# Performance work log

Measured on AMD Instinct MI355X. Metric: run time of the kernel, lower is better.

## Reference

```python
import jax, jax.numpy as jnp
import numpy as np

B, N, M = 2, 4096, 4096
QUERY_DIM, CONTEXT_DIM = 512, 768
H, D = 8, 64
INNER = H * D


def setup_inputs() -> dict:
    key = jax.random.key(0)
    ks = jax.random.split(key, 8)
    x = jax.random.normal(ks[0], (B, N, QUERY_DIM), dtype=jnp.float32)
    context_tensor = jax.random.normal(ks[1], (B, M, CONTEXT_DIM), dtype=jnp.float32)
    mask = jax.random.randint(ks[2], (B, M), 0, 2) > 0  # bool [B, M]
    s = 0.02
    Wq = jax.random.normal(ks[3], (QUERY_DIM, INNER), dtype=jnp.float32) * s
    Wk = jax.random.normal(ks[4], (CONTEXT_DIM, INNER), dtype=jnp.float32) * s
    Wv = jax.random.normal(ks[5], (CONTEXT_DIM, INNER), dtype=jnp.float32) * s
    Wo = jax.random.normal(ks[6], (INNER, QUERY_DIM), dtype=jnp.float32) * s
    bo = jnp.zeros((QUERY_DIM,), dtype=jnp.float32)
    return {"x": x, "context_tensor": context_tensor, "mask": mask,
            "Wq": Wq, "Wk": Wk, "Wv": Wv, "Wo": Wo, "bo": bo}


def reference(x, context_tensor, mask, Wq, Wk, Wv, Wo, bo):
    scale = D ** (-0.5)
    # projections -> [B, T, H, D]
    q = (x @ Wq).reshape(B, N, H, D)
    k = (context_tensor @ Wk).reshape(B, M, H, D)
    v = (context_tensor @ Wv).reshape(B, M, H, D)
    # scores [B, H, N, M]
    attn = jnp.einsum('bnhd,bmhd->bhnm', q, k) * scale
    neg = -jnp.finfo(attn.dtype).max
    attn = jnp.where(mask[:, None, None, :], attn, neg)
    attn = jax.nn.softmax(attn, axis=-1)
    out = jnp.einsum('bhnm,bmhd->bnhd', attn, v).reshape(B, N, INNER)
    return out @ Wo + bo  # dropout is 0.0 -> identity
```

## Files before the change

### kernel.cpp

```cpp
#include <hip/hip_runtime.h>

typedef unsigned short u16;
typedef unsigned int u32;
typedef __attribute__((ext_vector_type(8))) short bf16x8;
typedef __attribute__((ext_vector_type(4))) float f32x4;

#define CSC 0.1803368801111244f

__device__ __forceinline__ u16 f2b(float f) {
  union { float f; u32 u; } c; c.f = f;
  return (u16)((c.u + 0x8000u) >> 16);
}

__device__ __forceinline__ uint2 pk4(f32x4 p) {
  union { float f; u32 u; } c0, c1, c2, c3;
  c0.f = p[0]; c1.f = p[1]; c2.f = p[2]; c3.f = p[3];
  u32 a = c0.u + 0x8000u, b = c1.u + 0x8000u;
  u32 c = c2.u + 0x8000u, d = c3.u + 0x8000u;
  uint2 r;
  r.x = __builtin_amdgcn_perm(b, a, 0x07060302u);
  r.y = __builtin_amdgcn_perm(d, c, 0x07060302u);
  return r;
}

__device__ __forceinline__ void async16(const void* g, void* s) {
  __builtin_amdgcn_global_load_lds(
      (const __attribute__((address_space(1))) u32*)g,
      (__attribute__((address_space(3))) u32*)s, 16, 0, 0);
}

__global__ void prep(const float* __restrict__ x, const float* __restrict__ ctx,
                     const int* __restrict__ mask,
                     const float* __restrict__ Wq, const float* __restrict__ Wk,
                     const float* __restrict__ Wv, const float* __restrict__ Wo,
                     u16* __restrict__ Xb, u16* __restrict__ Cb, u16* __restrict__ mbb,
                     u16* __restrict__ Wtq, u16* __restrict__ Wtkv, u16* __restrict__ Wto) {
  const int bid = blockIdx.x, tid = threadIdx.x;
  if (bid < 10240) {
    const float* src; u16* dst; int i;
    if (bid < 4096) { i = (bid * 256 + tid) * 4; src = x; dst = Xb; }
    else { i = ((bid - 4096) * 256 + tid) * 4; src = ctx; dst = Cb; }
    float4 f = *(const float4*)&src[i];
    ushort4 o;
    o.x = f2b(f.x); o.y = f2b(f.y); o.z = f2b(f.z); o.w = f2b(f.w);
    *(ushort4*)&dst[i] = o;
  } else if (bid < 15360) {
    int t = bid - 10240;
    const float* W; u16* Wt; int Kd;
    if (t < 1024)      { W = Wq; Wt = Wtq; Kd = 512; }
    else if (t < 2560) { W = Wk; Wt = Wtkv; Kd = 768; t -= 1024; }
    else if (t < 4096) { W = Wv; Wt = Wtkv + (size_t)512 * 768; Kd = 768; t -= 2560; }
    else               { W = Wo; Wt = Wto; Kd = 512; t -= 4096; }
    int idx = t * 256 + tid;
    int n = idx / Kd, k = idx - n * Kd;
    Wt[idx] = f2b(W[(size_t)k * 512 + n]);
  } else {
    int i = (bid - 15360) * 256 + tid;
    mbb[i] = f2b(mask[i] ? 0.f : -1e30f);
  }
}

__global__ __launch_bounds__(256, 2)
void gemm_qkv(const u16* __restrict__ Xb, const u16* __restrict__ Cb,
              const u16* __restrict__ Wtq, const u16* __restrict__ Wtkv,
              u16* __restrict__ Qb, u16* __restrict__ Kb, u16* __restrict__ Vt) {
  __shared__ u16 As[128 * 64];
  __shared__ u16 Bs[128 * 64];
  const int tid = threadIdx.x;
  const int w = tid >> 6, lane = tid & 63, quad = lane >> 4, l16 = lane & 15;
  const int wr = w >> 1, wc = w & 1;
  const int y = blockIdx.y;
  const bool isQ = (y < 4);
  const u16* A  = isQ ? Xb : Cb;
  const u16* Bt = isQ ? Wtq : Wtkv;
  const int K   = isQ ? 512 : 768;
  const int n0  = isQ ? y * 128 : (y - 4) * 128;
  const size_t m0 = (size_t)blockIdx.x * 128;
  const u16* Ab = A + m0 * K;
  const u16* Bb = Bt + (size_t)n0 * K;

  const int cswz = (((lane & 7) ^ ((lane >> 3) & 7)) << 3);
  const int sw0 = ((quad ^ (l16 & 7)) << 3);
  const int sw1 = sw0 ^ 32;
  const int rA = w * 32 + (lane >> 3);

  f32x4 acc[4][4];
#pragma unroll
  for (int i = 0; i < 4; i++)
#pragma unroll
    for (int j = 0; j < 4; j++) acc[i][j] = (f32x4){0.f, 0.f, 0.f, 0.f};

  for (int k0 = 0; k0 < K; k0 += 64) {
#pragma unroll
    for (int t = 0; t < 4; t++) {
      async16(Ab + (size_t)(rA + t * 8) * K + k0 + cswz, &As[(w * 32 + t * 8) * 64]);
      async16(Bb + (size_t)(rA + t * 8) * K + k0 + cswz, &Bs[(w * 32 + t * 8) * 64]);
    }
    __syncthreads();
#pragma unroll
    for (int ks = 0; ks < 2; ks++) {
      const int so = ks ? sw1 : sw0;
      bf16x8 af[4], bfr[4];
#pragma unroll
      for (int i = 0; i < 4; i++) {
        af[i]  = *(const bf16x8*)&As[(wr * 64 + i * 16 + l16) * 64 + so];
        bfr[i] = *(const bf16x8*)&Bs[(wc * 64 + i * 16 + l16) * 64 + so];
      }
#pragma unroll
      for (int i = 0; i < 4; i++)
#pragma unroll
        for (int j = 0; j < 4; j++)
          acc[i][j] = __builtin_amdgcn_mfma_f32_16x16x32_bf16(af[i], bfr[j], acc[i][j], 0, 0, 0);
    }
    __syncthreads();
  }

  if (!isQ && n0 >= 512) {
#pragma unroll
    for (int i = 0; i < 4; i++)
#pragma unroll
      for (int j = 0; j < 4; j++) {
        size_t row0 = m0 + wr * 64 + i * 16 + quad * 4;
        int d = n0 - 512 + wc * 64 + j * 16 + l16;
        *(uint2*)&Vt[(size_t)d * 8192 + row0] = pk4(acc[i][j]);
      }
  } else {
    u16* C0 = isQ ? Qb : Kb;
#pragma unroll
    for (int i = 0; i < 4; i++)
#pragma unroll
      for (int j = 0; j < 4; j++)
#pragma unroll
        for (int r = 0; r < 4; r++) {
          size_t row = m0 + wr * 64 + i * 16 + quad * 4 + r;
          int col = n0 + wc * 64 + j * 16 + l16;
          C0[row * 512 + col] = f2b(acc[i][j][r]);
        }
  }
}

__global__ __launch_bounds__(256, 2)
void gemm_o(const u16* __restrict__ A, const u16* __restrict__ Bt,
            const float* __restrict__ bias, float* __restrict__ Cf) {
  __shared__ u16 As[64 * 64];
  __shared__ u16 Bs[128 * 64];
  const int tid = threadIdx.x;
  const int w = tid >> 6, lane = tid & 63, quad = lane >> 4, l16 = lane & 15;
  const int wr = w >> 1, wc = w & 1;
  const size_t m0 = (size_t)blockIdx.x * 64;
  const int n0 = blockIdx.y * 128;
  const u16* Ab = A + m0 * 512;
  const u16* Bb = Bt + (size_t)n0 * 512;

  const int cswz = (((lane & 7) ^ ((lane >> 3) & 7)) << 3);
  const int sw0 = ((quad ^ (l16 & 7)) << 3);
  const int sw1 = sw0 ^ 32;
  const int r8 = lane >> 3;

  f32x4 acc[2][4];
#pragma unroll
  for (int i = 0; i < 2; i++)
#pragma unroll
    for (int j = 0; j < 4; j++) acc[i][j] = (f32x4){0.f, 0.f, 0.f, 0.f};

  for (int k0 = 0; k0 < 512; k0 += 64) {
#pragma unroll
    for (int t = 0; t < 2; t++)
      async16(Ab + (size_t)(w * 16 + t * 8 + r8) * 512 + k0 + cswz, &As[(w * 16 + t * 8) * 64]);
#pragma unroll
    for (int t = 0; t < 4; t++)
      async16(Bb + (size_t)(w * 32 + t * 8 + r8) * 512 + k0 + cswz, &Bs[(w * 32 + t * 8) * 64]);
    __syncthreads();
#pragma unroll
    for (int ks = 0; ks < 2; ks++) {
      const int so = ks ? sw1 : sw0;
      bf16x8 af[2], bfr[4];
#pragma unroll
      for (int i = 0; i < 2; i++)
        af[i] = *(const bf16x8*)&As[(wr * 32 + i * 16 + l16) * 64 + so];
#pragma unroll
      for (int j = 0; j < 4; j++)
        bfr[j] = *(const bf16x8*)&Bs[(wc * 64 + j * 16 + l16) * 64 + so];
#pragma unroll
      for (int i = 0; i < 2; i++)
#pragma unroll
        for (int j = 0; j < 4; j++)
          acc[i][j] = __builtin_amdgcn_mfma_f32_16x16x32_bf16(af[i], bfr[j], acc[i][j], 0, 0, 0);
    }
    __syncthreads();
  }

#pragma unroll
  for (int i = 0; i < 2; i++)
#pragma unroll
    for (int j = 0; j < 4; j++)
#pragma unroll
      for (int r = 0; r < 4; r++) {
        size_t row = m0 + wr * 32 + i * 16 + quad * 4 + r;
        int col = n0 + wc * 64 + j * 16 + l16;
        Cf[row * 512 + col] = acc[i][j][r] + bias[col];
      }
}

__global__ __launch_bounds__(256, 2)
void attn_kernel(const u16* __restrict__ Q, const u16* __restrict__ Kg,
                 const u16* __restrict__ Vt, const u16* __restrict__ mbb,
                 u16* __restrict__ AO) {
  __shared__ u16 QPs[128 * 64];
  __shared__ u16 Ks[2][64 * 64];
  __shared__ u16 Vs[2][64 * 64];
  __shared__ u16 Mb[4096];

  const int tid = threadIdx.x;
  const int w = tid >> 6, lane = tid & 63, quad = lane >> 4, l16 = lane & 15;
  const int qb = blockIdx.x, h = blockIdx.y, b = blockIdx.z;
  const size_t qrow0 = (size_t)b * 4096 + (size_t)qb * 128;
  const size_t crow0 = (size_t)b * 4096;
  const int hcol = h * 64;

  const int cswz = (((lane & 7) ^ ((lane >> 3) & 7)) << 3);
  const int sw0 = ((quad ^ (l16 & 7)) << 3);
  const int sw1 = sw0 ^ 32;
  const int r8 = lane >> 3;

#pragma unroll
  for (int t = 0; t < 4; t++)
    async16(Q + (qrow0 + w * 32 + t * 8 + r8) * 512 + hcol + cswz, &QPs[(w * 32 + t * 8) * 64]);
  async16(Kg + (crow0 + w * 16 + r8) * 512 + hcol + cswz, &Ks[0][(w * 16) * 64]);
  async16(Kg + (crow0 + w * 16 + 8 + r8) * 512 + hcol + cswz, &Ks[0][(w * 16 + 8) * 64]);
  async16(Vt + (size_t)(hcol + w * 16 + r8) * 8192 + crow0 + cswz, &Vs[0][(w * 16) * 64]);
  async16(Vt + (size_t)(hcol + w * 16 + 8 + r8) * 8192 + crow0 + cswz, &Vs[0][(w * 16 + 8) * 64]);
#pragma unroll
  for (int t = 0; t < 2; t++) {
    int c = t * 4 + w;
    async16(mbb + (size_t)b * 4096 + c * 512 + lane * 8, &Mb[c * 512]);
  }
  __syncthreads();

  bf16x8 qf[2][2];
#pragma unroll
  for (int qt = 0; qt < 2; qt++) {
    qf[qt][0] = *(const bf16x8*)&QPs[(w * 32 + qt * 16 + l16) * 64 + sw0];
    qf[qt][1] = *(const bf16x8*)&QPs[(w * 32 + qt * 16 + l16) * 64 + sw1];
  }
  __asm volatile("s_waitcnt lgkmcnt(0)" ::: "memory");

  f32x4 Oacc[2][4];
#pragma unroll
  for (int qt = 0; qt < 2; qt++)
#pragma unroll
    for (int dt = 0; dt < 4; dt++) Oacc[qt][dt] = (f32x4){0.f, 0.f, 0.f, 0.f};
  float lsum[2] = {0.f, 0.f};

  for (int mt = 0; mt < 64; mt++) {
    const int cur = mt & 1;
    const size_t m0 = (size_t)mt * 64;

    if (mt < 63) {
      const size_t mn = m0 + 64;
      async16(Kg + (crow0 + mn + w * 16 + r8) * 512 + hcol + cswz, &Ks[cur ^ 1][(w * 16) * 64]);
      async16(Kg + (crow0 + mn + w * 16 + 8 + r8) * 512 + hcol + cswz, &Ks[cur ^ 1][(w * 16 + 8) * 64]);
      async16(Vt + (size_t)(hcol + w * 16 + r8) * 8192 + crow0 + mn + cswz, &Vs[cur ^ 1][(w * 16) * 64]);
      async16(Vt + (size_t)(hcol + w * 16 + 8 + r8) * 8192 + crow0 + mn + cswz, &Vs[cur ^ 1][(w * 16 + 8) * 64]);
    }

    f32x4 mv[4];
#pragma unroll
    for (int mtt = 0; mtt < 4; mtt++) {
      uint2 md = *(const uint2*)&Mb[m0 + mtt * 16 + quad * 4];
      union { u32 u; float f; } a0, a1, a2, a3;
      a0.u = md.x << 16; a1.u = md.x & 0xFFFF0000u;
      a2.u = md.y << 16; a3.u = md.y & 0xFFFF0000u;
      mv[mtt] = (f32x4){a0.f, a1.f, a2.f, a3.f};
    }

    f32x4 sacc[2][4];
#pragma unroll
    for (int qt = 0; qt < 2; qt++)
#pragma unroll
      for (int mtt = 0; mtt < 4; mtt++) sacc[qt][mtt] = (f32x4){0.f, 0.f, 0.f, 0.f};
#pragma unroll
    for (int ks = 0; ks < 2; ks++) {
      const int so = ks ? sw1 : sw0;
      bf16x8 kb[4];
#pragma unroll
      for (int mtt = 0; mtt < 4; mtt++)
        kb[mtt] = *(const bf16x8*)&Ks[cur][(mtt * 16 + l16) * 64 + so];
#pragma unroll
      for (int qt = 0; qt < 2; qt++)
#pragma unroll
        for (int mtt = 0; mtt < 4; mtt++)
          sacc[qt][mtt] = __builtin_amdgcn_mfma_f32_16x16x32_bf16(kb[mtt], qf[qt][ks], sacc[qt][mtt], 0, 0, 0);
    }

#pragma unroll
    for (int qt = 0; qt < 2; qt++) {
      const int q = w * 32 + qt * 16 + l16;
      float rs = 0.f;
#pragma unroll
      for (int mtt = 0; mtt < 4; mtt++) {
        f32x4 p;
#pragma unroll
        for (int r = 0; r < 4; r++) {
          p[r] = __builtin_amdgcn_exp2f(fmaf(sacc[qt][mtt][r], CSC, mv[mtt][r]));
          rs += p[r];
        }
        const int c = mtt * 2 + (quad >> 1);
        *(uint2*)&QPs[q * 64 + (((c ^ (q & 7)) << 3) | ((quad & 1) * 4))] = pk4(p);
      }
      lsum[qt] += rs;
    }

    __asm volatile("s_waitcnt lgkmcnt(0)" ::: "memory");

#pragma unroll
    for (int ks = 0; ks < 2; ks++) {
      const int so = ks ? sw1 : sw0;
      bf16x8 va[4], pb[2];
#pragma unroll
      for (int dt = 0; dt < 4; dt++)
        va[dt] = *(const bf16x8*)&Vs[cur][(dt * 16 + l16) * 64 + so];
#pragma unroll
      for (int qt = 0; qt < 2; qt++) {
        const int q = w * 32 + qt * 16 + l16;
        const int c = ks * 4 + quad;
        pb[qt] = *(const bf16x8*)&QPs[q * 64 + ((c ^ (q & 7)) << 3)];
      }
#pragma unroll
      for (int qt = 0; qt < 2; qt++)
#pragma unroll
        for (int dt = 0; dt < 4; dt++)
          Oacc[qt][dt] = __builtin_amdgcn_mfma_f32_16x16x32_bf16(va[dt], pb[qt], Oacc[qt][dt], 0, 0, 0);
    }
    __syncthreads();
  }

  float inv[2];
#pragma unroll
  for (int qt = 0; qt < 2; qt++) {
    float l = lsum[qt];
    l += __shfl_xor(l, 16);
    l += __shfl_xor(l, 32);
    inv[qt] = 1.0f / l;
  }

#pragma unroll
  for (int qt = 0; qt < 2; qt++)
#pragma unroll
    for (int dt = 0; dt < 4; dt++) {
      f32x4 o;
#pragma unroll
      for (int r = 0; r < 4; r++) o[r] = Oacc[qt][dt][r] * inv[qt];
      *(uint2*)&AO[(qrow0 + w * 32 + qt * 16 + l16) * 512 + hcol + dt * 16 + quad * 4] = pk4(o);
    }
}


extern "C" void kernel_launch(void* const* d_in, const int* in_sizes, int n_in,
                              void* d_out, int out_size, void* d_ws, size_t ws_size,
                              hipStream_t stream) {
  const float* x   = (const float*)d_in[0];
  const float* ctx = (const float*)d_in[1];
  const int*  mask = (const int*)d_in[2];
  const float* Wq  = (const float*)d_in[3];
  const float* Wk  = (const float*)d_in[4];
  const float* Wv  = (const float*)d_in[5];
  const float* Wo  = (const float*)d_in[6];
  const float* bo  = (const float*)d_in[7];
  float* out = (float*)d_out;

  char* p = (char*)d_ws;
  u16* Xb   = (u16*)p; p += (size_t)8192 * 512 * 2;
  u16* Cb   = (u16*)p; p += (size_t)8192 * 768 * 2;
  u16* Wtq  = (u16*)p; p += (size_t)512 * 512 * 2;
  u16* Wtkv = (u16*)p; p += (size_t)1024 * 768 * 2;
  u16* Wto  = (u16*)p; p += (size_t)512 * 512 * 2;
  u16* Qb   = (u16*)p; p += (size_t)8192 * 512 * 2;
  u16* Kb   = (u16*)p; p += (size_t)8192 * 512 * 2;
  u16* Vtg  = (u16*)p; p += (size_t)512 * 8192 * 2;
  u16* AOb  = (u16*)p; p += (size_t)8192 * 512 * 2;
  u16* mbb  = (u16*)p; p += (size_t)8192 * 2;

  prep<<<15392, 256, 0, stream>>>(x, ctx, mask, Wq, Wk, Wv, Wo,
                                  Xb, Cb, mbb, Wtq, Wtkv, Wto);
  gemm_qkv<<<dim3(64, 12), 256, 0, stream>>>(Xb, Cb, Wtq, Wtkv, Qb, Kb, Vtg);
  attn_kernel<<<dim3(32, 8, 2), 256, 0, stream>>>(Qb, Kb, Vtg, mbb, AOb);
  gemm_o<<<dim3(128, 4), 256, 0, stream>>>(AOb, Wto, bo, out);
}
```

Baseline: 254.4 us.

## Keep P in registers, tile weight transpose, fp32 mask, remap attention grid

The attention kernel no longer writes softmax probabilities to shared memory. It keeps them in registers as bf16x4 and feeds them straight into 16x16x16 MFMAs, which removes LDS round-trips and a wait per tile. Q fragments are now loaded directly from global memory. The mask is stored as fp32, which removes the bf16 unpacking. The weight transpose in prep now uses 64x64 LDS-tiled blocks with coalesced stores, and the attention grid is flattened so that heads and batches of the same query block are interleaved. The trade-off is twice as many, smaller MFMAs in the PV product and a larger fp32 mask buffer in LDS.

```diff
diff --git a/kernel.cpp b/kernel.cpp
--- a/kernel.cpp
+++ b/kernel.cpp
@@ -3,6 +3,7 @@
 typedef unsigned short u16;
 typedef unsigned int u32;
 typedef __attribute__((ext_vector_type(8))) short bf16x8;
+typedef __attribute__((ext_vector_type(4))) short bf16x4;
 typedef __attribute__((ext_vector_type(4))) float f32x4;
 
 #define CSC 0.1803368801111244f
@@ -23,6 +24,12 @@
   return r;
 }
 
+__device__ __forceinline__ bf16x4 pk4v(f32x4 p) {
+  union { uint2 u; bf16x4 v; } c;
+  c.u = pk4(p);
+  return c.v;
+}
+
 __device__ __forceinline__ void async16(const void* g, void* s) {
   __builtin_amdgcn_global_load_lds(
       (const __attribute__((address_space(1))) u32*)g,
@@ -33,8 +40,9 @@
                      const int* __restrict__ mask,
                      const float* __restrict__ Wq, const float* __restrict__ Wk,
                      const float* __restrict__ Wv, const float* __restrict__ Wo,
-                     u16* __restrict__ Xb, u16* __restrict__ Cb, u16* __restrict__ mbb,
+                     u16* __restrict__ Xb, u16* __restrict__ Cb, float* __restrict__ mbf,
                      u16* __restrict__ Wtq, u16* __restrict__ Wtkv, u16* __restrict__ Wto) {
+  __shared__ u16 Tl[64 * 65];
   const int bid = blockIdx.x, tid = threadIdx.x;
   if (bid < 10240) {
     const float* src; u16* dst; int i;
@@ -44,19 +52,38 @@
     ushort4 o;
     o.x = f2b(f.x); o.y = f2b(f.y); o.z = f2b(f.z); o.w = f2b(f.w);
     *(ushort4*)&dst[i] = o;
-  } else if (bid < 15360) {
+  } else if (bid < 10560) {
     int t = bid - 10240;
-    const float* W; u16* Wt; int Kd;
-    if (t < 1024)      { W = Wq; Wt = Wtq; Kd = 512; }
-    else if (t < 2560) { W = Wk; Wt = Wtkv; Kd = 768; t -= 1024; }
-    else if (t < 4096) { W = Wv; Wt = Wtkv + (size_t)512 * 768; Kd = 768; t -= 2560; }
-    else               { W = Wo; Wt = Wto; Kd = 512; t -= 4096; }
-    int idx = t * 256 + tid;
-    int n = idx / Kd, k = idx - n * Kd;
-    Wt[idx] = f2b(W[(size_t)k * 512 + n]);
+    const float* W; u16* Wt; int Kd, tt;
+    if (t < 64)       { W = Wq; Wt = Wtq;  Kd = 512; tt = t; }
+    else if (t < 160) { W = Wk; Wt = Wtkv; Kd = 768; tt = t - 64; }
+    else if (t < 256) { W = Wv; Wt = Wtkv + (size_t)512 * 768; Kd = 768; tt = t - 160; }
+    else              { W = Wo; Wt = Wto;  Kd = 512; tt = t - 256; }
+    const int k0 = (tt >> 3) * 64, n0 = (tt & 7) * 64;
+    {
+      const int r = tid >> 2, cg = (tid & 3) * 16;
+#pragma unroll
+      for (int i = 0; i < 4; i++) {
+        float4 f = *(const float4*)&W[(size_t)(k0 + r) * 512 + n0 + cg + i * 4];
+        Tl[r * 65 + cg + i * 4 + 0] = f2b(f.x);
+        Tl[r * 65 + cg + i * 4 + 1] = f2b(f.y);
+        Tl[r * 65 + cg + i * 4 + 2] = f2b(f.z);
+        Tl[r * 65 + cg + i * 4 + 3] = f2b(f.w);
+      }
+    }
+    __syncthreads();
+    {
+      const int n = tid >> 2, kg = (tid & 3) * 16;
+      u16 buf[16];
+#pragma unroll
+      for (int i = 0; i < 16; i++) buf[i] = Tl[(kg + i) * 65 + n];
+      u16* dst = &Wt[(size_t)(n0 + n) * Kd + k0 + kg];
+      *(uint4*)dst = *(const uint4*)&buf[0];
+      *(uint4*)(dst + 8) = *(const uint4*)&buf[8];
+    }
   } else {
-    int i = (bid - 15360) * 256 + tid;
-    mbb[i] = f2b(mask[i] ? 0.f : -1e30f);
+    int i = (bid - 10560) * 256 + tid;
+    mbf[i] = mask[i] ? 0.f : -1e30f;
   }
 }
 
@@ -204,16 +231,16 @@
 
 __global__ __launch_bounds__(256, 2)
 void attn_kernel(const u16* __restrict__ Q, const u16* __restrict__ Kg,
-                 const u16* __restrict__ Vt, const u16* __restrict__ mbb,
+                 const u16* __restrict__ Vt, const float* __restrict__ mbf,
                  u16* __restrict__ AO) {
-  __shared__ u16 QPs[128 * 64];
   __shared__ u16 Ks[2][64 * 64];
   __shared__ u16 Vs[2][64 * 64];
-  __shared__ u16 Mb[4096];
+  __shared__ float Mf[4096];
 
   const int tid = threadIdx.x;
   const int w = tid >> 6, lane = tid & 63, quad = lane >> 4, l16 = lane & 15;
-  const int qb = blockIdx.x, h = blockIdx.y, b = blockIdx.z;
+  const int l = blockIdx.x;
+  const int qb = l >> 4, hb = l & 15, h = hb >> 1, b = hb & 1;
   const size_t qrow0 = (size_t)b * 4096 + (size_t)qb * 128;
   const size_t crow0 = (size_t)b * 4096;
   const int hcol = h * 64;
@@ -223,27 +250,23 @@
   const int sw1 = sw0 ^ 32;
   const int r8 = lane >> 3;
 
-#pragma unroll
-  for (int t = 0; t < 4; t++)
-    async16(Q + (qrow0 + w * 32 + t * 8 + r8) * 512 + hcol + cswz, &QPs[(w * 32 + t * 8) * 64]);
+  bf16x8 qf[2][2];
+#pragma unroll
+  for (int qt = 0; qt < 2; qt++)
+#pragma unroll
+    for (int ks = 0; ks < 2; ks++)
+      qf[qt][ks] = *(const bf16x8*)&Q[(qrow0 + w * 32 + qt * 16 + l16) * 512 + hcol + ks * 32 + quad * 8];
+
   async16(Kg + (crow0 + w * 16 + r8) * 512 + hcol + cswz, &Ks[0][(w * 16) * 64]);
   async16(Kg + (crow0 + w * 16 + 8 + r8) * 512 + hcol + cswz, &Ks[0][(w * 16 + 8) * 64]);
   async16(Vt + (size_t)(hcol + w * 16 + r8) * 8192 + crow0 + cswz, &Vs[0][(w * 16) * 64]);
   async16(Vt + (size_t)(hcol + w * 16 + 8 + r8) * 8192 + crow0 + cswz, &Vs[0][(w * 16 + 8) * 64]);
 #pragma unroll
-  for (int t = 0; t < 2; t++) {
-    int c = t * 4 + w;
-    async16(mbb + (size_t)b * 4096 + c * 512 + lane * 8, &Mb[c * 512]);
+  for (int t = 0; t < 4; t++) {
+    int i = w * 4 + t;
+    async16(mbf + crow0 + i * 256 + lane * 4, &Mf[i * 256]);
   }
   __syncthreads();
-
-  bf16x8 qf[2][2];
-#pragma unroll
-  for (int qt = 0; qt < 2; qt++) {
-    qf[qt][0] = *(const bf16x8*)&QPs[(w * 32 + qt * 16 + l16) * 64 + sw0];
-    qf[qt][1] = *(const bf16x8*)&QPs[(w * 32 + qt * 16 + l16) * 64 + sw1];
-  }
-  __asm volatile("s_waitcnt lgkmcnt(0)" ::: "memory");
 
   f32x4 Oacc[2][4];
 #pragma unroll
@@ -266,13 +289,8 @@
 
     f32x4 mv[4];
 #pragma unroll
-    for (int mtt = 0; mtt < 4; mtt++) {
-      uint2 md = *(const uint2*)&Mb[m0 + mtt * 16 + quad * 4];
-      union { u32 u; float f; } a0, a1, a2, a3;
-      a0.u = md.x << 16; a1.u = md.x & 0xFFFF0000u;
-      a2.u = md.y << 16; a3.u = md.y & 0xFFFF0000u;
-      mv[mtt] = (f32x4){a0.f, a1.f, a2.f, a3.f};
-    }
+    for (int mtt = 0; mtt < 4; mtt++)
+      mv[mtt] = *(const f32x4*)&Mf[m0 + mtt * 16 + quad * 4];
 
     f32x4 sacc[2][4];
 #pragma unroll
@@ -293,9 +311,9 @@
           sacc[qt][mtt] = __builtin_amdgcn_mfma_f32_16x16x32_bf16(kb[mtt], qf[qt][ks], sacc[qt][mtt], 0, 0, 0);
     }
 
+    bf16x4 pf[2][4];
 #pragma unroll
     for (int qt = 0; qt < 2; qt++) {
-      const int q = w * 32 + qt * 16 + l16;
       float rs = 0.f;
 #pragma unroll
       for (int mtt = 0; mtt < 4; mtt++) {
@@ -305,32 +323,23 @@
           p[r] = __builtin_amdgcn_exp2f(fmaf(sacc[qt][mtt][r], CSC, mv[mtt][r]));
           rs += p[r];
         }
-        const int c = mtt * 2 + (quad >> 1);
-        *(uint2*)&QPs[q * 64 + (((c ^ (q & 7)) << 3) | ((quad & 1) * 4))] = pk4(p);
+        pf[qt][mtt] = pk4v(p);
       }
       lsum[qt] += rs;
     }
 
-    __asm volatile("s_waitcnt lgkmcnt(0)" ::: "memory");
-
-#pragma unroll
-    for (int ks = 0; ks < 2; ks++) {
-      const int so = ks ? sw1 : sw0;
-      bf16x8 va[4], pb[2];
+#pragma unroll
+    for (int mtt = 0; mtt < 4; mtt++) {
+      bf16x4 va[4];
 #pragma unroll
       for (int dt = 0; dt < 4; dt++)
-        va[dt] = *(const bf16x8*)&Vs[cur][(dt * 16 + l16) * 64 + so];
-#pragma unroll
-      for (int qt = 0; qt < 2; qt++) {
-        const int q = w * 32 + qt * 16 + l16;
-        const int c = ks * 4 + quad;
-        pb[qt] = *(const bf16x8*)&QPs[q * 64 + ((c ^ (q & 7)) << 3)];
-      }
+        va[dt] = *(const bf16x4*)&Vs[cur][(dt * 16 + l16) * 64 +
+                    (((mtt * 2 + (quad >> 1)) ^ (l16 & 7)) << 3) + ((quad & 1) << 2)];
 #pragma unroll
       for (int qt = 0; qt < 2; qt++)
 #pragma unroll
         for (int dt = 0; dt < 4; dt++)
-          Oacc[qt][dt] = __builtin_amdgcn_mfma_f32_16x16x32_bf16(va[dt], pb[qt], Oacc[qt][dt], 0, 0, 0);
+          Oacc[qt][dt] = __builtin_amdgcn_mfma_f32_16x16x16bf16_1k(va[dt], pf[qt][mtt], Oacc[qt][dt], 0, 0, 0);
     }
     __syncthreads();
   }
@@ -338,10 +347,10 @@
   float inv[2];
 #pragma unroll
   for (int qt = 0; qt < 2; qt++) {
-    float l = lsum[qt];
-    l += __shfl_xor(l, 16);
-    l += __shfl_xor(l, 32);
-    inv[qt] = 1.0f / l;
+    float lv = lsum[qt];
+    lv += __shfl_xor(lv, 16);
+    lv += __shfl_xor(lv, 32);
+    inv[qt] = 1.0f / lv;
   }
 
 #pragma unroll
@@ -379,11 +388,11 @@
   u16* Kb   = (u16*)p; p += (size_t)8192 * 512 * 2;
   u16* Vtg  = (u16*)p; p += (size_t)512 * 8192 * 2;
   u16* AOb  = (u16*)p; p += (size_t)8192 * 512 * 2;
-  u16* mbb  = (u16*)p; p += (size_t)8192 * 2;
-
-  prep<<<15392, 256, 0, stream>>>(x, ctx, mask, Wq, Wk, Wv, Wo,
-                                  Xb, Cb, mbb, Wtq, Wtkv, Wto);
+  float* mbf = (float*)p; p += (size_t)8192 * 4;
+
+  prep<<<10592, 256, 0, stream>>>(x, ctx, mask, Wq, Wk, Wv, Wo,
+                                  Xb, Cb, mbf, Wtq, Wtkv, Wto);
   gemm_qkv<<<dim3(64, 12), 256, 0, stream>>>(Xb, Cb, Wtq, Wtkv, Qb, Kb, Vtg);
-  attn_kernel<<<dim3(32, 8, 2), 256, 0, stream>>>(Qb, Kb, Vtg, mbb, AOb);
+  attn_kernel<<<512, 256, 0, stream>>>(Qb, Kb, Vtg, mbf, AOb);
   gemm_o<<<dim3(128, 4), 256, 0, stream>>>(AOb, Wto, bo, out);
 }
```

New measurement: 240.9 us. -5.3%, faster.
